# Performance work log

Hardware: AMD Instinct MI355X
Metric: run time of the kernel (lower is better)

## Reference

```python
import jax, jax.numpy as jnp
import numpy as np

B, S, DIM = 2, 4096, 1024
H, DH = 16, 64
M = 256  # number of random features (rmfa_config['num_feats'])
EPS = 1e-6


def setup_inputs() -> dict:
    key = jax.random.key(0)
    ks = jax.random.split(key, 10)
    s_in = 1.0 / np.sqrt(DIM)
    inp = {
        "X": jax.random.normal(ks[0], (B, S, DIM), dtype=jnp.float32),
        "mask": jnp.ones((B, S), dtype=jnp.float32),
        "Wq": jax.random.normal(ks[1], (DIM, H * DH), dtype=jnp.float32) * s_in,
        "bq": jnp.zeros((H * DH,), dtype=jnp.float32),
        "Wk": jax.random.normal(ks[2], (DIM, H * DH), dtype=jnp.float32) * s_in,
        "bk": jnp.zeros((H * DH,), dtype=jnp.float32),
        "Wv": jax.random.normal(ks[3], (DIM, H * DH), dtype=jnp.float32) * s_in,
        "bv": jnp.zeros((H * DH,), dtype=jnp.float32),
        "Wf": jax.random.normal(ks[4], (H * DH, DIM), dtype=jnp.float32) * s_in,
        "bf": jnp.zeros((DIM,), dtype=jnp.float32),
        "proj": jax.random.normal(ks[5], (DH, M), dtype=jnp.float32),  # random-feature projection (frozen)
    }
    return inp


def _split_heads(x):  # [B,S,H*DH] -> [B,H,S,DH]
    return x.reshape(B, S, H, DH).transpose(0, 2, 1, 3)


def _pre_sbn(x):
    # PreSBN: project onto unit sphere (required for Schoenberg-kernel random features)
    return x / (jnp.linalg.norm(x, axis=-1, keepdims=True) + EPS)


def _phi(x, proj):
    # positive random features of the (Schoenberg/exponential) kernel on the sphere
    # x: [B,H,S,DH] unit-norm -> phi: [B,H,S,M]
    u = jnp.einsum('bhsd,dm->bhsm', x, proj)
    # ||x||^2 = 1 after pre-norm, so the -||x||^2/2 correction is a constant -0.5
    return jnp.exp(u - 0.5) / np.sqrt(M)


def reference(X, mask, Wq, bq, Wk, bk, Wv, bv, Wf, bf, proj):
    Q = _split_heads(X @ Wq + bq)
    K = _split_heads(X @ Wk + bk)
    V = _split_heads(X @ Wv + bv)
    Q = _pre_sbn(Q)
    K = _pre_sbn(K)
    # kernelized (linear) attention in fp32
    phiQ = _phi(Q.astype(jnp.float32), proj)
    phiK = _phi(K.astype(jnp.float32), proj) * mask[:, None, :, None]
    KV = jnp.einsum('bhsm,bhsd->bhmd', phiK, V.astype(jnp.float32))  # [B,H,M,DH]
    Z = phiK.sum(axis=2)                                             # [B,H,M]
    num = jnp.einsum('bhsm,bhmd->bhsd', phiQ, KV)
    den = jnp.einsum('bhsm,bhm->bhs', phiQ, Z) + EPS
    attn = num / den[..., None]
    # PostSBN(d_model=DIM//H=DH): restore scale removed by the sphere projection
    attn = attn * np.sqrt(DH)
    attn = attn.transpose(0, 2, 1, 3).reshape(B, S, H * DH)  # combine heads
    return attn @ Wf + bf
```

## Files before the change

kernel.cpp:

```cpp
#include <hip/hip_runtime.h>
#include <cmath>

typedef unsigned short u16;
typedef unsigned int   u32;
typedef __attribute__((ext_vector_type(8))) short bf16x8;
typedef __attribute__((ext_vector_type(4))) float f32x4;

#define DEV __device__ __forceinline__
#define MFMA(a,b,c) __builtin_amdgcn_mfma_f32_16x16x32_bf16((a),(b),(c),0,0,0)

#define GLOAD16(dst, src) __builtin_amdgcn_global_load_lds( \
    (const __attribute__((address_space(1))) void*)(src), \
    (__attribute__((address_space(3))) void*)(dst), 16, 0, 0)

DEV u16 f2bf(float x){ union{float f;u32 u;} v; v.f=x; u32 r=v.u+0x7FFFu+((v.u>>16)&1u); return (u16)(r>>16); }
DEV float bf2f(u16 h){ union{u32 u;float f;} v; v.u=((u32)h)<<16; return v.f; }

DEV int swz(int row, int cb){ return row*64 + ((cb ^ (row&7))*8); }

#define STGU(arr, slotsz, slot, j, P, k0) GLOAD16( \
    &(arr)[(slot)*(slotsz) + ((j)*64 + w*8)*64], \
    (P) + (size_t)((j)*64 + srow_)*1024 + (k0) + scol_)

#define GEMM_CORE_128x256(As, Bs, Ap, Bp, acc) do{ \
    const int srow_ = w*8 + (l>>3); \
    const int scol_ = ((l&7) ^ (l>>3))*8; \
    STGU(Bs,256*64,0,0,Bp,0); STGU(Bs,256*64,0,1,Bp,0); STGU(Bs,256*64,0,2,Bp,0); \
    STGU(Bs,256*64,0,3,Bp,0); STGU(As,128*64,0,0,Ap,0); STGU(As,128*64,0,1,Ap,0); \
    STGU(Bs,256*64,1,0,Bp,64); STGU(Bs,256*64,1,1,Bp,64); STGU(Bs,256*64,1,2,Bp,64); \
    STGU(Bs,256*64,1,3,Bp,64); STGU(As,128*64,1,0,Ap,64); STGU(As,128*64,1,1,Ap,64); \
    asm volatile("s_waitcnt vmcnt(6)" ::: "memory"); \
    __builtin_amdgcn_s_barrier(); \
    __builtin_amdgcn_sched_barrier(0); \
    for(int kt=0; kt<16; ++kt){ \
        const int sl = kt % 3; \
        const int st = (kt+2) % 3; \
        const int k2 = (kt+2)*64; \
        const u16* Asl = (As) + sl*(128*64); \
        const u16* Bsl = (Bs) + sl*(256*64); \
        bf16x8 bf_[4][2], af_[4][2]; \
        _Pragma("unroll") \
        for(int nt=0;nt<4;++nt) \
            _Pragma("unroll") \
            for(int ks=0;ks<2;++ks) \
                bf_[nt][ks] = *(const bf16x8*)&Bsl[swz(64*wc+16*nt+c, 4*ks+g)]; \
        _Pragma("unroll") \
        for(int mt=0;mt<4;++mt) \
            _Pragma("unroll") \
            for(int ks=0;ks<2;++ks) \
                af_[mt][ks] = *(const bf16x8*)&Asl[swz(64*wr+16*mt+c, 4*ks+g)]; \
        if (kt<=13){ STGU(Bs,256*64,st,0,Bp,k2); STGU(Bs,256*64,st,1,Bp,k2); STGU(Bs,256*64,st,2,Bp,k2); \
                     STGU(Bs,256*64,st,3,Bp,k2); STGU(As,128*64,st,0,Ap,k2); STGU(As,128*64,st,1,Ap,k2); } \
        _Pragma("unroll") \
        for(int mt=0;mt<4;++mt) \
            _Pragma("unroll") \
            for(int nt=0;nt<4;++nt) \
                _Pragma("unroll") \
                for(int ks=0;ks<2;++ks) \
                    acc[mt][nt] = MFMA(af_[mt][ks], bf_[nt][ks], acc[mt][nt]); \
        if (kt<=13)      { asm volatile("s_waitcnt vmcnt(6)" ::: "memory"); } \
        else if (kt==14) { asm volatile("s_waitcnt vmcnt(0)" ::: "memory"); } \
        __builtin_amdgcn_s_barrier(); \
        __builtin_amdgcn_sched_barrier(0); \
    } \
}while(0)

__global__ __launch_bounds__(256) void k_prep(const float* __restrict__ X,
        const float* __restrict__ Wq, const float* __restrict__ Wk,
        const float* __restrict__ Wv, const float* __restrict__ Wf,
        const float* __restrict__ proj,
        u16* __restrict__ Xb, u16* __restrict__ WT, u16* __restrict__ Wfh,
        u16* __restrict__ pPh){
    const int bid = blockIdx.x, tid = threadIdx.x;
    if (bid < 4096){
        __shared__ float t[32][33];
        const int which = bid >> 10, bb = bid & 1023;
        const float* in = (which==0) ? Wq : (which==1) ? Wk : (which==2) ? Wv : Wf;
        u16* hi = (which==3) ? Wfh : (WT + (size_t)which*1048576);
        const int r0 = (bb>>5)*32, c0 = (bb&31)*32;
        const int lr = tid>>3, lc = (tid&7)*4;
        float4 v = *(const float4*)(in + (size_t)(r0+lr)*1024 + c0 + lc);
        t[lr][lc]=v.x; t[lr][lc+1]=v.y; t[lr][lc+2]=v.z; t[lr][lc+3]=v.w;
        __syncthreads();
        ushort4 o;
        o.x=f2bf(t[lc+0][lr]); o.y=f2bf(t[lc+1][lr]);
        o.z=f2bf(t[lc+2][lr]); o.w=f2bf(t[lc+3][lr]);
        *(ushort4*)(hi + (size_t)(c0+lr)*1024 + r0+lc) = o;
    } else if (bid < 12288){
        size_t i = ((size_t)(bid-4096)*256 + tid)*4;
        float4 v = *(const float4*)(X+i);
        ushort4 o; o.x=f2bf(v.x); o.y=f2bf(v.y); o.z=f2bf(v.z); o.w=f2bf(v.w);
        *(ushort4*)(Xb+i) = o;
    } else {
        int idx = (bid-12288)*256 + tid;
        int e = idx&7, l = (idx>>3)&63, f = idx>>9;
        int nt = f>>1, ks = f&1;
        int d = 32*ks + 8*(l>>4) + e;
        int m = 16*nt + (l&15);
        pPh[idx] = f2bf(proj[d*256 + m]);
    }
}

__global__ __launch_bounds__(512,2) void k_qkv(const u16* __restrict__ Xb, const u16* __restrict__ WT,
        const float* __restrict__ bq, const float* __restrict__ bk, const float* __restrict__ bv,
        u16* __restrict__ Qb, u16* __restrict__ Kb, u16* __restrict__ VT){
    __shared__ u16 As[3*128*64];
    __shared__ u16 Bs[3*256*64];
    const int bx = blockIdx.x, y = blockIdx.y;
    const int wsel = y>>2, nb = y&3;
    const int tid = threadIdx.x, w = tid>>6, l = tid&63, g = l>>4, c = l&15;
    const int wr = w>>2, wc = w&3;
    const u16* Ap = Xb + (size_t)bx*128*1024;
    const u16* Bp = WT + (size_t)wsel*1048576 + (size_t)nb*256*1024;
    f32x4 acc[4][4];
    #pragma unroll
    for(int mt=0;mt<4;++mt)
        #pragma unroll
        for(int nt=0;nt<4;++nt) acc[mt][nt] = f32x4{0.f,0.f,0.f,0.f};

    GEMM_CORE_128x256(As, Bs, Ap, Bp, acc);

    const int n0 = nb*256 + 64*wc;
    const int b = bx>>5;
    if (wsel < 2){
        u16* Out = wsel ? Kb : Qb;
        const float* bias = wsel ? bk : bq;
        float bb[4];
        #pragma unroll
        for(int nt=0;nt<4;++nt) bb[nt] = bias[n0+16*nt+c];
        #pragma unroll
        for(int mt=0;mt<4;++mt){
            #pragma unroll
            for(int nt=0;nt<4;++nt)
                #pragma unroll
                for(int r=0;r<4;++r) acc[mt][nt][r] += bb[nt];
            #pragma unroll
            for(int r=0;r<4;++r){
                float ss = 0.f;
                #pragma unroll
                for(int nt=0;nt<4;++nt){ float vv = acc[mt][nt][r]; ss += vv*vv; }
                ss += __shfl_xor(ss,1); ss += __shfl_xor(ss,2);
                ss += __shfl_xor(ss,4); ss += __shfl_xor(ss,8);
                float sc = 1.f/(sqrtf(ss)+1e-6f);
                #pragma unroll
                for(int nt=0;nt<4;++nt) acc[mt][nt][r] *= sc;
            }
            const int rowb = bx*128 + 64*wr + 16*mt + 4*g;
            #pragma unroll
            for(int nt=0;nt<4;++nt)
                #pragma unroll
                for(int r=0;r<4;++r)
                    Out[(size_t)(rowb+r)*1024 + n0 + 16*nt + c] = f2bf(acc[mt][nt][r]);
        }
    } else {
        const int h = nb*4 + wc;
        float bb[4];
        #pragma unroll
        for(int nt=0;nt<4;++nt) bb[nt] = bv[n0+16*nt+c];
        #pragma unroll
        for(int mt=0;mt<4;++mt)
            #pragma unroll
            for(int nt=0;nt<4;++nt){
                const int d = 16*nt + c;
                const int s0m = (bx&31)*128 + 64*wr + 16*mt + 4*g;
                ushort4 o;
                o.x = f2bf(acc[mt][nt][0]+bb[nt]); o.y = f2bf(acc[mt][nt][1]+bb[nt]);
                o.z = f2bf(acc[mt][nt][2]+bb[nt]); o.w = f2bf(acc[mt][nt][3]+bb[nt]);
                *(ushort4*)(VT + ((size_t)(b*16+h)*64 + d)*4096 + s0m) = o;
            }
    }
}

__global__ __launch_bounds__(512) void k_kv(const u16* __restrict__ Kb,
        const u16* __restrict__ pPh,
        const float* __restrict__ mask, const u16* __restrict__ VT,
        float* __restrict__ KVpart, float* __restrict__ Zpart){
    __shared__ u16 pps[16384];
    __shared__ u16 phiT[256][136];
    __shared__ u16 Vs[64][136];
    __shared__ float zbuf[8][256];
    const int chunk = blockIdx.x, bh = blockIdx.y;
    const int b = bh>>4, h = bh&15;
    const int tid = threadIdx.x, w = tid>>6, l = tid&63, g = l>>4, c = l&15;
    #pragma unroll
    for(int j2=0;j2<4;++j2){
        const int base = (j2*8 + w)*512;
        GLOAD16(pps + base, pPh + base + l*8);
    }
    f32x4 kv[2][4];
    #pragma unroll
    for(int mt=0;mt<2;++mt) for(int dt=0;dt<4;++dt) kv[mt][dt] = f32x4{0.f,0.f,0.f,0.f};
    float zacc[16];
    #pragma unroll
    for(int nt=0;nt<16;++nt) zacc[nt]=0.f;
    const int vd = tid>>3, vs8 = (tid&7)*16;
    asm volatile("s_waitcnt vmcnt(0)" ::: "memory");
    __syncthreads();
    for(int t=0;t<4;++t){
        const int s0 = chunk*512 + t*128;
        {
            const u16* pv = VT + ((size_t)bh*64 + vd)*4096 + s0 + vs8;
            uint4 v0 = *(const uint4*)pv, v1 = *(const uint4*)(pv+8);
            *(uint4*)&Vs[vd][vs8] = v0; *(uint4*)&Vs[vd][vs8+8] = v1;
        }
        f32x4 ph[16];
        #pragma unroll
        for(int nt=0;nt<16;++nt) ph[nt] = f32x4{0.f,0.f,0.f,0.f};
        #pragma unroll
        for(int ks=0;ks<2;++ks){
            const int srow = s0 + 16*w + c;
            bf16x8 ah = *(const bf16x8*)(Kb + (size_t)(b*4096+srow)*1024 + h*64 + 32*ks + 8*g);
            #pragma unroll
            for(int nt=0;nt<16;++nt){
                bf16x8 bh8 = *(const bf16x8*)(pps + ((nt*2+ks)*64 + l)*8);
                ph[nt] = MFMA(ah, bh8, ph[nt]);
            }
        }
        float mk[4];
        #pragma unroll
        for(int r=0;r<4;++r) mk[r] = mask[b*4096 + s0 + 16*w + 4*g + r];
        #pragma unroll
        for(int nt=0;nt<16;++nt){
            float zs = 0.f;
            #pragma unroll
            for(int r=0;r<4;++r){
                float phv = __expf(ph[nt][r]-0.5f)*0.0625f*mk[r];
                phiT[c+16*nt][16*w+4*g+r] = f2bf(phv);
                zs += phv;
            }
            zacc[nt] += zs;
        }
        __syncthreads();
        #pragma unroll
        for(int ks=0;ks<4;++ks){
            bf16x8 afr[2], bfr[4];
            #pragma unroll
            for(int mt=0;mt<2;++mt) afr[mt] = *(const bf16x8*)&phiT[32*w+16*mt+c][32*ks+8*g];
            #pragma unroll
            for(int dt=0;dt<4;++dt) bfr[dt] = *(const bf16x8*)&Vs[16*dt+c][32*ks+8*g];
            #pragma unroll
            for(int mt=0;mt<2;++mt)
                #pragma unroll
                for(int dt=0;dt<4;++dt)
                    kv[mt][dt] = MFMA(afr[mt], bfr[dt], kv[mt][dt]);
        }
        __syncthreads();
    }
    #pragma unroll
    for(int nt=0;nt<16;++nt){
        float z = zacc[nt];
        z += __shfl_xor(z,16); z += __shfl_xor(z,32);
        if (g==0) zbuf[w][c+16*nt] = z;
    }
    __syncthreads();
    if (tid < 256){
        float z = 0.f;
        #pragma unroll
        for(int ww=0;ww<8;++ww) z += zbuf[ww][tid];
        Zpart[((size_t)bh*8+chunk)*256 + tid] = z;
    }
    float* kout = KVpart + ((size_t)bh*8+chunk)*16384;
    #pragma unroll
    for(int mt=0;mt<2;++mt)
        #pragma unroll
        for(int dt=0;dt<4;++dt)
            #pragma unroll
            for(int r=0;r<4;++r)
                kout[(32*w+16*mt+4*g+r)*64 + 16*dt + c] = kv[mt][dt][r];
}

__global__ __launch_bounds__(256) void k_kvreduce(const float* __restrict__ KVpart,
        const float* __restrict__ Zpart, u16* __restrict__ KVT, float* __restrict__ Z){
    const int gid = blockIdx.x*256 + threadIdx.x;
    const int bh = gid >> 12;
    const int i0 = (gid & 4095) * 4;
    float4 s = {0.f,0.f,0.f,0.f};
    const float* base = KVpart + (size_t)bh*8*16384 + i0;
    #pragma unroll
    for(int ch=0; ch<8; ++ch){
        float4 v = *(const float4*)(base + (size_t)ch*16384);
        s.x+=v.x; s.y+=v.y; s.z+=v.z; s.w+=v.w;
    }
    const int m = i0 >> 6, d = i0 & 63;
    u16* dst = KVT + ((size_t)bh*64 + d)*256 + m;
    dst[0]   = f2bf(s.x);
    dst[256] = f2bf(s.y);
    dst[512] = f2bf(s.z);
    dst[768] = f2bf(s.w);
    if (gid < 8192){
        const int zbh = gid >> 8, zm = gid & 255;
        float z = 0.f;
        #pragma unroll
        for(int ch=0; ch<8; ++ch) z += Zpart[((size_t)zbh*8+ch)*256 + zm];
        Z[zbh*256 + zm] = z;
    }
}

__global__ __launch_bounds__(512) void k_attn(const u16* __restrict__ Qb,
        const u16* __restrict__ pPh,
        const u16* __restrict__ KVT, const float* __restrict__ Z, u16* __restrict__ attn){
    __shared__ u16 kvs[64*256];
    __shared__ u16 pps[16384];
    __shared__ u16 phi[128][264];
    __shared__ float Zs[256];
    const int bx = blockIdx.x, bh = blockIdx.y;
    const int b = bh>>4, h = bh&15;
    const int tid = threadIdx.x, w = tid>>6, l = tid&63, g = l>>4, c = l&15;
    if (tid < 256) Zs[tid] = Z[bh*256 + tid];
    #pragma unroll
    for(int j2=0;j2<4;++j2){
        const int base_row = (j2*8 + w)*2;
        const int row = base_row + (l>>5), cb = l&31;
        GLOAD16(kvs + base_row*256,
                KVT + (size_t)bh*16384 + row*256 + ((cb ^ (row&7))*8));
    }
    #pragma unroll
    for(int j2=0;j2<4;++j2){
        const int base = (j2*8 + w)*512;
        GLOAD16(pps + base, pPh + base + l*8);
    }
    asm volatile("s_waitcnt vmcnt(0)" ::: "memory");
    __syncthreads();

    for(int t=0;t<4;++t){
        const int s0 = bx*512 + t*128;
        f32x4 ph[16];
        #pragma unroll
        for(int nt=0;nt<16;++nt) ph[nt] = f32x4{0.f,0.f,0.f,0.f};
        #pragma unroll
        for(int ks=0;ks<2;++ks){
            const int srow = s0 + 16*w + c;
            bf16x8 ah = *(const bf16x8*)(Qb + (size_t)(b*4096+srow)*1024 + h*64 + 32*ks + 8*g);
            #pragma unroll
            for(int nt=0;nt<16;++nt){
                bf16x8 bh8 = *(const bf16x8*)(pps + ((nt*2+ks)*64 + l)*8);
                ph[nt] = MFMA(ah, bh8, ph[nt]);
            }
        }
        float den[4] = {0.f,0.f,0.f,0.f};
        #pragma unroll
        for(int nt=0;nt<16;++nt){
            float zv = Zs[c+16*nt];
            #pragma unroll
            for(int r=0;r<4;++r){
                float phv = __expf(ph[nt][r]-0.5f)*0.0625f;
                den[r] += phv*zv;
                phi[16*w+4*g+r][c+16*nt] = f2bf(phv);
            }
        }
        #pragma unroll
        for(int r=0;r<4;++r){
            den[r] += __shfl_xor(den[r],1); den[r] += __shfl_xor(den[r],2);
            den[r] += __shfl_xor(den[r],4); den[r] += __shfl_xor(den[r],8);
            den[r] += 1e-6f;
        }
        __syncthreads();
        f32x4 nm[4];
        #pragma unroll
        for(int dt=0;dt<4;++dt) nm[dt] = f32x4{0.f,0.f,0.f,0.f};
        #pragma unroll
        for(int j=0;j<8;++j){
            bf16x8 af = *(const bf16x8*)&phi[16*w+c][32*j+8*g];
            #pragma unroll
            for(int dt=0;dt<4;++dt){
                const int row = 16*dt + c, cb = 4*j + g;
                bf16x8 bfr = *(const bf16x8*)(kvs + row*256 + ((cb ^ (row&7))*8));
                nm[dt] = MFMA(af, bfr, nm[dt]);
            }
        }
        #pragma unroll
        for(int dt=0;dt<4;++dt)
            #pragma unroll
            for(int r=0;r<4;++r){
                const int srow = s0 + 16*w + 4*g + r;
                attn[(size_t)(b*4096+srow)*1024 + h*64 + 16*dt + c] = f2bf(nm[dt][r]*8.f/den[r]);
            }
        __syncthreads();
    }
}

__global__ __launch_bounds__(512,2) void k_out(const u16* __restrict__ attn,
        const u16* __restrict__ Wh, const float* __restrict__ bfb, float* __restrict__ out){
    __shared__ u16 As[3*128*64];
    __shared__ u16 Bs[3*256*64];
    const int bx = blockIdx.x, by = blockIdx.y;
    const int tid = threadIdx.x, w = tid>>6, l = tid&63, g = l>>4, c = l&15;
    const int wr = w>>2, wc = w&3;
    const u16* Ap = attn + (size_t)bx*128*1024;
    const u16* Bp = Wh + (size_t)by*256*1024;
    f32x4 acc[4][4];
    #pragma unroll
    for(int mt=0;mt<4;++mt)
        #pragma unroll
        for(int nt=0;nt<4;++nt) acc[mt][nt] = f32x4{0.f,0.f,0.f,0.f};

    GEMM_CORE_128x256(As, Bs, Ap, Bp, acc);

    const int n0 = by*256 + 64*wc;
    #pragma unroll
    for(int mt=0;mt<4;++mt){
        const int rowb = bx*128 + 64*wr + 16*mt + 4*g;
        #pragma unroll
        for(int nt=0;nt<4;++nt){
            const float bb = bfb[n0+16*nt+c];
            #pragma unroll
            for(int r=0;r<4;++r)
                out[(size_t)(rowb+r)*1024 + n0 + 16*nt + c] = acc[mt][nt][r] + bb;
        }
    }
}

extern "C" void kernel_launch(void* const* d_in, const int* in_sizes, int n_in,
                              void* d_out, int out_size, void* d_ws, size_t ws_size,
                              hipStream_t stream){
    (void)in_sizes; (void)n_in; (void)out_size;
    const float* X    = (const float*)d_in[0];
    const float* mask = (const float*)d_in[1];
    const float* Wq   = (const float*)d_in[2];
    const float* bq   = (const float*)d_in[3];
    const float* Wk   = (const float*)d_in[4];
    const float* bk   = (const float*)d_in[5];
    const float* Wv   = (const float*)d_in[6];
    const float* bv   = (const float*)d_in[7];
    const float* Wf   = (const float*)d_in[8];
    const float* bfb  = (const float*)d_in[9];
    const float* proj = (const float*)d_in[10];
    float* out = (float*)d_out;

    char* w = (char*)d_ws;
    size_t off = 0;
    auto alloc = [&](size_t n)->void*{ void* p = w + off; off = (off + n + 255) & ~(size_t)255; return p; };
    u16*   Xb     = (u16*)  alloc((size_t)8192*1024*2);
    u16*   WT     = (u16*)  alloc((size_t)3*1048576*2);
    u16*   Wfh    = (u16*)  alloc((size_t)1048576*2);
    u16*   pPh    = (u16*)  alloc(16384*2);
    u16*   Qb     = (u16*)  alloc((size_t)8192*1024*2);
    u16*   Kb     = (u16*)  alloc((size_t)8192*1024*2);
    u16*   VT     = (u16*)  alloc((size_t)32*64*4096*2);
    float* KVpart = (float*)alloc((size_t)32*8*16384*4);
    float* Zpart  = (float*)alloc((size_t)32*8*256*4);
    u16*   KVT    = (u16*)  alloc((size_t)32*64*256*2);
    float* Zr     = (float*)alloc((size_t)32*256*4);
    u16*   attnB  = (u16*)  alloc((size_t)8192*1024*2);
    if (off > ws_size) return;

    k_prep<<<dim3(12352), 256, 0, stream>>>(X, Wq, Wk, Wv, Wf, proj, Xb, WT, Wfh, pPh);
    k_qkv<<<dim3(64,12), 512, 0, stream>>>(Xb, WT, bq, bk, bv, Qb, Kb, VT);
    k_kv<<<dim3(8,32), 512, 0, stream>>>(Kb, pPh, mask, VT, KVpart, Zpart);
    k_kvreduce<<<dim3(512), 256, 0, stream>>>(KVpart, Zpart, KVT, Zr);
    k_attn<<<dim3(8,32), 512, 0, stream>>>(Qb, pPh, KVT, Zr, attnB);
    k_out<<<dim3(64,4), 512, 0, stream>>>(attnB, Wfh, bfb, out);
}
```

Baseline: 157.5 us.

## Enlarge QKV GEMM tile to 256x256 with double-buffered LDS pipeline

Replaces the 128x256 three-stage GEMM core in the QKV projection kernel with an inline 256x256 tile. Each wave now computes 128 rows, the LDS pipeline is double-buffered, and the grid is halved to 32x12 blocks. The bigger tile is meant to raise arithmetic intensity and cut redundant loads of the weight tile. In exchange it doubles accumulator registers under launch_bounds(512,2), may spill or lower occupancy, leaves only 384 blocks for the CUs, and drops one pipeline stage of latency hiding.

```diff
diff --git a/kernel.cpp b/kernel.cpp
--- a/kernel.cpp
+++ b/kernel.cpp
@@ -104,24 +104,63 @@
 __global__ __launch_bounds__(512,2) void k_qkv(const u16* __restrict__ Xb, const u16* __restrict__ WT,
         const float* __restrict__ bq, const float* __restrict__ bk, const float* __restrict__ bv,
         u16* __restrict__ Qb, u16* __restrict__ Kb, u16* __restrict__ VT){
-    __shared__ u16 As[3*128*64];
-    __shared__ u16 Bs[3*256*64];
+    __shared__ u16 As[2*256*64];
+    __shared__ u16 Bs[2*256*64];
     const int bx = blockIdx.x, y = blockIdx.y;
     const int wsel = y>>2, nb = y&3;
     const int tid = threadIdx.x, w = tid>>6, l = tid&63, g = l>>4, c = l&15;
     const int wr = w>>2, wc = w&3;
-    const u16* Ap = Xb + (size_t)bx*128*1024;
+    const u16* Ap = Xb + (size_t)bx*256*1024;
     const u16* Bp = WT + (size_t)wsel*1048576 + (size_t)nb*256*1024;
-    f32x4 acc[4][4];
-    #pragma unroll
-    for(int mt=0;mt<4;++mt)
+    const int srow_ = w*8 + (l>>3);
+    const int scol_ = ((l&7) ^ (l>>3))*8;
+    f32x4 acc[8][4];
+    #pragma unroll
+    for(int mt=0;mt<8;++mt)
         #pragma unroll
         for(int nt=0;nt<4;++nt) acc[mt][nt] = f32x4{0.f,0.f,0.f,0.f};
-
-    GEMM_CORE_128x256(As, Bs, Ap, Bp, acc);
-
+    STGU(Bs,256*64,0,0,Bp,0); STGU(Bs,256*64,0,1,Bp,0);
+    STGU(Bs,256*64,0,2,Bp,0); STGU(Bs,256*64,0,3,Bp,0);
+    STGU(As,256*64,0,0,Ap,0); STGU(As,256*64,0,1,Ap,0);
+    STGU(As,256*64,0,2,Ap,0); STGU(As,256*64,0,3,Ap,0);
+    asm volatile("s_waitcnt vmcnt(0)" ::: "memory");
+    __builtin_amdgcn_s_barrier();
+    __builtin_amdgcn_sched_barrier(0);
+    for(int kt=0; kt<16; ++kt){
+        const int cur = kt&1, nx = cur^1, k2 = (kt+1)*64;
+        const bool more = kt < 15;
+        const u16* Asl = As + cur*(256*64);
+        const u16* Bsl = Bs + cur*(256*64);
+        bf16x8 bf_[4][2];
+        #pragma unroll
+        for(int nt=0;nt<4;++nt)
+            #pragma unroll
+            for(int ks=0;ks<2;++ks)
+                bf_[nt][ks] = *(const bf16x8*)&Bsl[swz(64*wc+16*nt+c, 4*ks+g)];
+        if (more){
+            STGU(Bs,256*64,nx,0,Bp,k2); STGU(Bs,256*64,nx,1,Bp,k2);
+            STGU(Bs,256*64,nx,2,Bp,k2); STGU(Bs,256*64,nx,3,Bp,k2);
+            STGU(As,256*64,nx,0,Ap,k2); STGU(As,256*64,nx,1,Ap,k2);
+            STGU(As,256*64,nx,2,Ap,k2); STGU(As,256*64,nx,3,Ap,k2);
+        }
+        __builtin_amdgcn_s_setprio(1);
+        #pragma unroll
+        for(int mt=0;mt<8;++mt){
+            bf16x8 a0 = *(const bf16x8*)&Asl[swz(128*wr+16*mt+c, g)];
+            bf16x8 a1 = *(const bf16x8*)&Asl[swz(128*wr+16*mt+c, 4+g)];
+            #pragma unroll
+            for(int nt=0;nt<4;++nt){
+                acc[mt][nt] = MFMA(a0, bf_[nt][0], acc[mt][nt]);
+                acc[mt][nt] = MFMA(a1, bf_[nt][1], acc[mt][nt]);
+            }
+        }
+        __builtin_amdgcn_s_setprio(0);
+        if (more) asm volatile("s_waitcnt vmcnt(0)" ::: "memory");
+        __builtin_amdgcn_s_barrier();
+        __builtin_amdgcn_sched_barrier(0);
+    }
     const int n0 = nb*256 + 64*wc;
-    const int b = bx>>5;
+    const int b = bx>>4;
     if (wsel < 2){
         u16* Out = wsel ? Kb : Qb;
         const float* bias = wsel ? bk : bq;
@@ -129,7 +168,7 @@
         #pragma unroll
         for(int nt=0;nt<4;++nt) bb[nt] = bias[n0+16*nt+c];
         #pragma unroll
-        for(int mt=0;mt<4;++mt){
+        for(int mt=0;mt<8;++mt){
             #pragma unroll
             for(int nt=0;nt<4;++nt)
                 #pragma unroll
@@ -145,7 +184,7 @@
                 #pragma unroll
                 for(int nt=0;nt<4;++nt) acc[mt][nt][r] *= sc;
             }
-            const int rowb = bx*128 + 64*wr + 16*mt + 4*g;
+            const int rowb = bx*256 + 128*wr + 16*mt + 4*g;
             #pragma unroll
             for(int nt=0;nt<4;++nt)
                 #pragma unroll
@@ -158,11 +197,11 @@
         #pragma unroll
         for(int nt=0;nt<4;++nt) bb[nt] = bv[n0+16*nt+c];
         #pragma unroll
-        for(int mt=0;mt<4;++mt)
+        for(int mt=0;mt<8;++mt)
             #pragma unroll
             for(int nt=0;nt<4;++nt){
                 const int d = 16*nt + c;
-                const int s0m = (bx&31)*128 + 64*wr + 16*mt + 4*g;
+                const int s0m = (bx&15)*256 + 128*wr + 16*mt + 4*g;
                 ushort4 o;
                 o.x = f2bf(acc[mt][nt][0]+bb[nt]); o.y = f2bf(acc[mt][nt][1]+bb[nt]);
                 o.z = f2bf(acc[mt][nt][2]+bb[nt]); o.w = f2bf(acc[mt][nt][3]+bb[nt]);
@@ -445,7 +484,7 @@
     if (off > ws_size) return;
 
     k_prep<<<dim3(12352), 256, 0, stream>>>(X, Wq, Wk, Wv, Wf, proj, Xb, WT, Wfh, pPh);
-    k_qkv<<<dim3(64,12), 512, 0, stream>>>(Xb, WT, bq, bk, bv, Qb, Kb, VT);
+    k_qkv<<<dim3(32,12), 512, 0, stream>>>(Xb, WT, bq, bk, bv, Qb, Kb, VT);
     k_kv<<<dim3(8,32), 512, 0, stream>>>(Kb, pPh, mask, VT, KVpart, Zpart);
     k_kvreduce<<<dim3(512), 256, 0, stream>>>(KVpart, Zpart, KVT, Zr);
     k_attn<<<dim3(8,32), 512, 0, stream>>>(Qb, pPh, KVT, Zr, attnB);
```

Measured after the change: 171.0 us. +8.6%, slower.
